# Performance work log

Hardware: AMD Instinct MI355X
Metric: run time of the kernel (lower is better)

The kernel has to match this reference:

```python
import jax, jax.numpy as jnp
import numpy as np

B, S, T = 8, 2048, 128  # batch, seq_len, token_embedding_dim (== dep_transformed_dim, required by source bug)


def setup_inputs() -> dict:
    key = jax.random.key(0)
    k1, k2, k3, k4, k5, k6, k7 = jax.random.split(key, 7)
    sT = 1.0 / np.sqrt(T)
    sS = 1.0 / np.sqrt(S)
    return {
        "token_embeddings": jax.random.normal(k1, (B, S, T), jnp.float32),
        "dep_embeddings": jax.random.normal(k2, (B, S, T), jnp.float32),  # dead input (source bug), kept for fidelity
        "dep_heads": jax.random.randint(k3, (B, S), 0, S, jnp.int32),
        # composition_transform = Bilinear(T, T, T): weight [T_out, T_in1, T_in2], bias [T_out]
        "W_comp": jax.random.uniform(k4, (T, T, T), jnp.float32, -sT, sT),
        "b_comp": jax.random.uniform(k5, (T,), jnp.float32, -sT, sT),
        # reduction_transform = Linear(S, 1)
        "w_red": jax.random.uniform(k6, (1, S), jnp.float32, -sS, sS),
        "b_red": jax.random.uniform(k7, (1,), jnp.float32, -sS, sS),
    }


def reference(token_embeddings, dep_embeddings, dep_heads, W_comp, b_comp, w_red, b_red):
    # Faithful to source semantics (including the bug where dep_transform output is
    # discarded and tanh is applied to token_embeddings instead):
    #   dense[b,i,j,:] = tanh( bilinear(token[b,j], mask(i==heads[b,j]) * tanh(token[b,j])) )
    #   out[b,i,t]     = sum_j w_red[j] * dense[b,i,j,t] + b_red
    # Where mask is zero, bilinear collapses to its bias, so we never materialize
    # the [B,S,S,T] tensor: compute the 'active' value per token j and scatter-add
    # the delta vs. the bias-only baseline into row i = dep_heads[b,j].
    h = jnp.tanh(token_embeddings)                                   # [B,S,T]
    val = jnp.einsum('bsp,tpq,bsq->bst', token_embeddings, W_comp, h) + b_comp  # [B,S,T]
    act = jnp.tanh(val)                                              # active (masked-in) values
    base_val = jnp.tanh(b_comp)                                      # [T] value where mask is zero
    w = w_red[0]                                                     # [S], reduction weights over j
    base = jnp.sum(w) * base_val + b_red[0]                          # [T] bias-only row
    delta = w[None, :, None] * (act - base_val)                      # [B,S,T]
    b_idx = jnp.arange(token_embeddings.shape[0])[:, None]           # [B,1]
    out = base + jnp.zeros_like(act).at[b_idx, dep_heads].add(delta) # scatter over head rows
    return out
```

## Files before the change

kernel.cpp:

```cpp
#include <hip/hip_runtime.h>
#include <hip/hip_fp16.h>
#include <math.h>

#define S_LEN 2048
#define T_DIM 128
#define BM 128
#define TN 32
#define NBLK 512
#define TOKR 132

typedef _Float16 half8 __attribute__((ext_vector_type(8)));
typedef _Float16 half4 __attribute__((ext_vector_type(4)));
typedef float floatx16 __attribute__((ext_vector_type(16)));

__global__ __launch_bounds__(256) void prep_kernel(
    const float* __restrict__ W, const float* __restrict__ w_red,
    const float* __restrict__ b_comp, const float* __restrict__ b_red,
    _Float16* __restrict__ W16f, float* __restrict__ out) {
  const int blk = blockIdx.x;
  const int tid = threadIdx.x;
  if (blk < 256) {
    const int t = blk >> 1, qh = blk & 1;
    const int tc = t >> 5, tl = t & 31;
#pragma unroll
    for (int it = 0; it < 4; ++it) {
      const int e8 = it * 256 + tid;
      const int p = e8 >> 3;
      const int q = qh * 64 + (e8 & 7) * 8;
      const float* src = W + (size_t)t * 16384 + (size_t)p * 128 + q;
      const float4 v0 = *(const float4*)src;
      const float4 v1 = *(const float4*)(src + 4);
      half8 h;
      h[0] = (_Float16)v0.x; h[1] = (_Float16)v0.y;
      h[2] = (_Float16)v0.z; h[3] = (_Float16)v0.w;
      h[4] = (_Float16)v1.x; h[5] = (_Float16)v1.y;
      h[6] = (_Float16)v1.z; h[7] = (_Float16)v1.w;
      const int kc = q >> 4, lh2 = (q >> 3) & 1;
      *(half8*)(W16f + ((size_t)((p * 4 + tc) * 8 + kc)) * 512 + lh2 * 256 + tl * 8) = h;
    }
  } else {
    __shared__ float red4[4];
    float part = 0.f;
#pragma unroll
    for (int i = 0; i < 8; ++i) part += w_red[tid * 8 + i];
#pragma unroll
    for (int off = 32; off > 0; off >>= 1) part += __shfl_down(part, off, 64);
    if ((tid & 63) == 0) red4[tid >> 6] = part;
    __syncthreads();
    const float Sw = red4[0] + red4[1] + red4[2] + red4[3];
    const float br = b_red[0];
    const size_t base = (size_t)(blk - 256) * 1024 + (size_t)tid * 4;
    const int t0 = (int)(base & 127);
    float4 v;
    v.x = Sw * tanhf(b_comp[t0 + 0]) + br;
    v.y = Sw * tanhf(b_comp[t0 + 1]) + br;
    v.z = Sw * tanhf(b_comp[t0 + 2]) + br;
    v.w = Sw * tanhf(b_comp[t0 + 3]) + br;
    *(float4*)(out + base) = v;
  }
}

__global__ __launch_bounds__(512, 4) void main_kernel(
    const float* __restrict__ tok, const int* __restrict__ heads,
    const _Float16* __restrict__ W16f, const float* __restrict__ b_comp,
    const float* __restrict__ w_red, float* __restrict__ out) {
  __shared__ _Float16 tokT2[128 * TOKR];
  __shared__ float red[2][128 * TN];

  const int tid = threadIdx.x;
  const int lane = tid & 63;
  const int kh = tid >> 6;
  const int l31 = lane & 31;
  const int lh = lane >> 5;
  const int blk = blockIdx.x;
  const int tq = (blk >> 1) & 3;
  const int mb = ((blk >> 3) << 1) | (blk & 1);
  const size_t tokbase = (size_t)mb * BM * T_DIM;

#pragma unroll
  for (int it = 0; it < 8; ++it) {
    const int f = it * 512 + tid;
    const int m = f >> 5;
    const int p0 = (f & 31) * 4;
    const float4 v = *(const float4*)(tok + tokbase + (size_t)m * 128 + p0);
    const int mi = (m & 31) * 4 + (m >> 5);
    tokT2[(p0 + 0) * TOKR + mi] = (_Float16)v.x;
    tokT2[(p0 + 1) * TOKR + mi] = (_Float16)v.y;
    tokT2[(p0 + 2) * TOKR + mi] = (_Float16)v.z;
    tokT2[(p0 + 3) * TOKR + mi] = (_Float16)v.w;
  }

  half8 h16[4];
#pragma unroll
  for (int mh = 0; mh < 4; ++mh) {
    const int m = mh * 32 + l31;
    const int q0 = kh * 16 + lh * 8;
    const float4 v0 = *(const float4*)(tok + tokbase + (size_t)m * 128 + q0);
    const float4 v1 = *(const float4*)(tok + tokbase + (size_t)m * 128 + q0 + 4);
    h16[mh][0] = (_Float16)tanhf(v0.x);
    h16[mh][1] = (_Float16)tanhf(v0.y);
    h16[mh][2] = (_Float16)tanhf(v0.z);
    h16[mh][3] = (_Float16)tanhf(v0.w);
    h16[mh][4] = (_Float16)tanhf(v1.x);
    h16[mh][5] = (_Float16)tanhf(v1.y);
    h16[mh][6] = (_Float16)tanhf(v1.z);
    h16[mh][7] = (_Float16)tanhf(v1.w);
  }
  __syncthreads();

  const int off0 = ((tq * 8 + kh) << 9) + lane * 8;

  floatx16 acc[4];
#pragma unroll
  for (int mh = 0; mh < 4; ++mh)
#pragma unroll
    for (int r = 0; r < 16; ++r) acc[mh][r] = 0.f;

  half8 bf0, bf1, bf2;
  half4 tk0, tk1, tk2;

  auto loadB = [&](half8& bf, int p) {
    bf = *(const half8*)(W16f + (size_t)p * 16384 + off0);
  };
  auto loadT = [&](half4& tk, int p) {
    tk = *(const half4*)(tokT2 + p * TOKR + l31 * 4);
  };

  auto compute = [&](half8 bf, half4 tk) {
    half8 a0 = h16[0] * tk[0];
    half8 a1 = h16[1] * tk[1];
    half8 a2 = h16[2] * tk[2];
    half8 a3 = h16[3] * tk[3];
    acc[0] = __builtin_amdgcn_mfma_f32_32x32x16_f16(a0, bf, acc[0], 0, 0, 0);
    acc[1] = __builtin_amdgcn_mfma_f32_32x32x16_f16(a1, bf, acc[1], 0, 0, 0);
    acc[2] = __builtin_amdgcn_mfma_f32_32x32x16_f16(a2, bf, acc[2], 0, 0, 0);
    acc[3] = __builtin_amdgcn_mfma_f32_32x32x16_f16(a3, bf, acc[3], 0, 0, 0);
  };

  loadB(bf0, 0);  loadT(tk0, 0);
  loadB(bf1, 1);  loadT(tk1, 1);
  for (int p = 0; p < 126; p += 3) {
    loadB(bf2, p + 2);  loadT(tk2, p + 2);
    compute(bf0, tk0);
    loadB(bf0, p + 3);  loadT(tk0, p + 3);
    compute(bf1, tk1);
    loadB(bf1, p + 4);  loadT(tk1, p + 4);
    compute(bf2, tk2);
  }
  compute(bf0, tk0);
  compute(bf1, tk1);

  __syncthreads();
  {
    float* R = &red[kh & 1][0];
    const int g = kh >> 1;
#pragma unroll
    for (int phase = 0; phase < 4; ++phase) {
      if (g == phase) {
#pragma unroll
        for (int mh = 0; mh < 4; ++mh)
#pragma unroll
          for (int r = 0; r < 16; ++r) {
            const int m_loc = (r & 3) + 8 * (r >> 2) + 4 * lh;
            const int addr = (mh * 32 + m_loc) * TN + l31;
            if (phase == 0) R[addr] = acc[mh][r];
            else            R[addr] += acc[mh][r];
          }
      }
      __syncthreads();
    }
  }

  const int t_loc = tid & 31;
  const int mgrp = tid >> 5;
  const int t = tq * 32 + t_loc;
  const float bc = b_comp[t];
  const float tb = tanhf(bc);
#pragma unroll 4
  for (int mi = 0; mi < 8; ++mi) {
    const int m_loc = mi * 16 + mgrp;
    const int gm = mb * BM + m_loc;
    const int head = heads[gm];
    const float wr = w_red[gm & 2047];
    const float v = red[0][m_loc * TN + t_loc] + red[1][m_loc * TN + t_loc] + bc;
    atomicAdd(out + ((size_t)(gm >> 11) * S_LEN + head) * T_DIM + t,
              wr * (tanhf(v) - tb));
  }
}

extern "C" void kernel_launch(void* const* d_in, const int* in_sizes, int n_in,
                              void* d_out, int out_size, void* d_ws, size_t ws_size,
                              hipStream_t stream) {
  const float* tok    = (const float*)d_in[0];
  const int*   heads  = (const int*)d_in[2];
  const float* W      = (const float*)d_in[3];
  const float* b_comp = (const float*)d_in[4];
  const float* w_red  = (const float*)d_in[5];
  const float* b_red  = (const float*)d_in[6];
  float* out = (float*)d_out;

  _Float16* W16f = (_Float16*)d_ws;

  prep_kernel<<<2304, 256, 0, stream>>>(W, w_red, b_comp, b_red, W16f, out);
  main_kernel<<<NBLK, 512, 0, stream>>>(tok, heads, W16f, b_comp, w_red, out);
}
```

Baseline: 158.7 us.

## Use fast tanh, split weight conversion across more blocks, deepen MFMA prefetch

Replaces tanhf with an exp-based fast tanh built from __expf and __fdividef. Spreads the fp16 weight conversion over four times as many blocks, each handling one slice instead of looping four times. Deepens the software prefetch in the MFMA main loop from three to four buffers. Together these target transcendental cost, prep-kernel parallelism and load latency, at the price of slightly lower tanh accuracy and more register pressure.

```diff
diff --git a/kernel.cpp b/kernel.cpp
--- a/kernel.cpp
+++ b/kernel.cpp
@@ -13,31 +13,34 @@
 typedef _Float16 half4 __attribute__((ext_vector_type(4)));
 typedef float floatx16 __attribute__((ext_vector_type(16)));
 
+__device__ __forceinline__ float tanh_fast(float x) {
+  return 1.0f - __fdividef(2.0f, 1.0f + __expf(2.0f * x));
+}
+
 __global__ __launch_bounds__(256) void prep_kernel(
     const float* __restrict__ W, const float* __restrict__ w_red,
     const float* __restrict__ b_comp, const float* __restrict__ b_red,
     _Float16* __restrict__ W16f, float* __restrict__ out) {
   const int blk = blockIdx.x;
   const int tid = threadIdx.x;
-  if (blk < 256) {
-    const int t = blk >> 1, qh = blk & 1;
+  if (blk < 1024) {
+    const int t = blk >> 3;
+    const int qh = (blk >> 2) & 1;
+    const int it = blk & 3;
     const int tc = t >> 5, tl = t & 31;
-#pragma unroll
-    for (int it = 0; it < 4; ++it) {
-      const int e8 = it * 256 + tid;
-      const int p = e8 >> 3;
-      const int q = qh * 64 + (e8 & 7) * 8;
-      const float* src = W + (size_t)t * 16384 + (size_t)p * 128 + q;
-      const float4 v0 = *(const float4*)src;
-      const float4 v1 = *(const float4*)(src + 4);
-      half8 h;
-      h[0] = (_Float16)v0.x; h[1] = (_Float16)v0.y;
-      h[2] = (_Float16)v0.z; h[3] = (_Float16)v0.w;
-      h[4] = (_Float16)v1.x; h[5] = (_Float16)v1.y;
-      h[6] = (_Float16)v1.z; h[7] = (_Float16)v1.w;
-      const int kc = q >> 4, lh2 = (q >> 3) & 1;
-      *(half8*)(W16f + ((size_t)((p * 4 + tc) * 8 + kc)) * 512 + lh2 * 256 + tl * 8) = h;
-    }
+    const int e8 = it * 256 + tid;
+    const int p = e8 >> 3;
+    const int q = qh * 64 + (e8 & 7) * 8;
+    const float* src = W + (size_t)t * 16384 + (size_t)p * 128 + q;
+    const float4 v0 = *(const float4*)src;
+    const float4 v1 = *(const float4*)(src + 4);
+    half8 h;
+    h[0] = (_Float16)v0.x; h[1] = (_Float16)v0.y;
+    h[2] = (_Float16)v0.z; h[3] = (_Float16)v0.w;
+    h[4] = (_Float16)v1.x; h[5] = (_Float16)v1.y;
+    h[6] = (_Float16)v1.z; h[7] = (_Float16)v1.w;
+    const int kc = q >> 4, lh2 = (q >> 3) & 1;
+    *(half8*)(W16f + ((size_t)((p * 4 + tc) * 8 + kc)) * 512 + lh2 * 256 + tl * 8) = h;
   } else {
     __shared__ float red4[4];
     float part = 0.f;
@@ -49,13 +52,13 @@
     __syncthreads();
     const float Sw = red4[0] + red4[1] + red4[2] + red4[3];
     const float br = b_red[0];
-    const size_t base = (size_t)(blk - 256) * 1024 + (size_t)tid * 4;
+    const size_t base = (size_t)(blk - 1024) * 1024 + (size_t)tid * 4;
     const int t0 = (int)(base & 127);
     float4 v;
-    v.x = Sw * tanhf(b_comp[t0 + 0]) + br;
-    v.y = Sw * tanhf(b_comp[t0 + 1]) + br;
-    v.z = Sw * tanhf(b_comp[t0 + 2]) + br;
-    v.w = Sw * tanhf(b_comp[t0 + 3]) + br;
+    v.x = Sw * tanh_fast(b_comp[t0 + 0]) + br;
+    v.y = Sw * tanh_fast(b_comp[t0 + 1]) + br;
+    v.z = Sw * tanh_fast(b_comp[t0 + 2]) + br;
+    v.w = Sw * tanh_fast(b_comp[t0 + 3]) + br;
     *(float4*)(out + base) = v;
   }
 }
@@ -97,14 +100,14 @@
     const int q0 = kh * 16 + lh * 8;
     const float4 v0 = *(const float4*)(tok + tokbase + (size_t)m * 128 + q0);
     const float4 v1 = *(const float4*)(tok + tokbase + (size_t)m * 128 + q0 + 4);
-    h16[mh][0] = (_Float16)tanhf(v0.x);
-    h16[mh][1] = (_Float16)tanhf(v0.y);
-    h16[mh][2] = (_Float16)tanhf(v0.z);
-    h16[mh][3] = (_Float16)tanhf(v0.w);
-    h16[mh][4] = (_Float16)tanhf(v1.x);
-    h16[mh][5] = (_Float16)tanhf(v1.y);
-    h16[mh][6] = (_Float16)tanhf(v1.z);
-    h16[mh][7] = (_Float16)tanhf(v1.w);
+    h16[mh][0] = (_Float16)tanh_fast(v0.x);
+    h16[mh][1] = (_Float16)tanh_fast(v0.y);
+    h16[mh][2] = (_Float16)tanh_fast(v0.z);
+    h16[mh][3] = (_Float16)tanh_fast(v0.w);
+    h16[mh][4] = (_Float16)tanh_fast(v1.x);
+    h16[mh][5] = (_Float16)tanh_fast(v1.y);
+    h16[mh][6] = (_Float16)tanh_fast(v1.z);
+    h16[mh][7] = (_Float16)tanh_fast(v1.w);
   }
   __syncthreads();
 
@@ -116,8 +119,8 @@
 #pragma unroll
     for (int r = 0; r < 16; ++r) acc[mh][r] = 0.f;
 
-  half8 bf0, bf1, bf2;
-  half4 tk0, tk1, tk2;
+  half8 bf0, bf1, bf2, bf3;
+  half4 tk0, tk1, tk2, tk3;
 
   auto loadB = [&](half8& bf, int p) {
     bf = *(const half8*)(W16f + (size_t)p * 16384 + off0);
@@ -139,16 +142,22 @@
 
   loadB(bf0, 0);  loadT(tk0, 0);
   loadB(bf1, 1);  loadT(tk1, 1);
-  for (int p = 0; p < 126; p += 3) {
-    loadB(bf2, p + 2);  loadT(tk2, p + 2);
+  loadB(bf2, 2);  loadT(tk2, 2);
+  for (int p = 0; p < 124; p += 4) {
+    loadB(bf3, p + 3);  loadT(tk3, p + 3);
     compute(bf0, tk0);
-    loadB(bf0, p + 3);  loadT(tk0, p + 3);
+    loadB(bf0, p + 4);  loadT(tk0, p + 4);
     compute(bf1, tk1);
-    loadB(bf1, p + 4);  loadT(tk1, p + 4);
+    loadB(bf1, p + 5);  loadT(tk1, p + 5);
     compute(bf2, tk2);
-  }
+    loadB(bf2, p + 6);  loadT(tk2, p + 6);
+    compute(bf3, tk3);
+  }
+  loadB(bf3, 127);  loadT(tk3, 127);
   compute(bf0, tk0);
   compute(bf1, tk1);
+  compute(bf2, tk2);
+  compute(bf3, tk3);
 
   __syncthreads();
   {
@@ -175,7 +184,7 @@
   const int mgrp = tid >> 5;
   const int t = tq * 32 + t_loc;
   const float bc = b_comp[t];
-  const float tb = tanhf(bc);
+  const float tb = tanh_fast(bc);
 #pragma unroll 4
   for (int mi = 0; mi < 8; ++mi) {
     const int m_loc = mi * 16 + mgrp;
@@ -184,7 +193,7 @@
     const float wr = w_red[gm & 2047];
     const float v = red[0][m_loc * TN + t_loc] + red[1][m_loc * TN + t_loc] + bc;
     atomicAdd(out + ((size_t)(gm >> 11) * S_LEN + head) * T_DIM + t,
-              wr * (tanhf(v) - tb));
+              wr * (tanh_fast(v) - tb));
   }
 }
 
@@ -201,6 +210,6 @@
 
   _Float16* W16f = (_Float16*)d_ws;
 
-  prep_kernel<<<2304, 256, 0, stream>>>(W, w_red, b_comp, b_red, W16f, out);
+  prep_kernel<<<3072, 256, 0, stream>>>(W, w_red, b_comp, b_red, W16f, out);
   main_kernel<<<NBLK, 512, 0, stream>>>(tok, heads, W16f, b_comp, w_red, out);
 }
```

Result: no change. 159.0 us (+0.2%).
